# Kernel tuning notes

Measured on AMD Instinct MI355X. Metric: run time of the kernel, lower is better.

The kernel has to match this reference:

```python
import jax, jax.numpy as jnp
import numpy as np

NUM_CLASSES = 80
ANCHORS = np.array([[10,13],[16,30],[33,23],[30,61],[62,45],[59,119],[116,90],[156,198],[373,326]], np.float32)
MASK = [[0,1,2],[3,4,5],[6,7,8]]
STRIDES = [8, 16, 32]
MAX_OUT = 100      # max_output_size_per_class == max_total_size
IOU_THR = 0.45
SCORE_THR = 0.25
NMS_TOPK = 128     # per-class candidate pre-selection for greedy NMS (>= MAX_OUT)


def setup_inputs() -> dict:
    key = jax.random.key(0)
    k1, k2, k3 = jax.random.split(key, 3)
    B = 16
    C = 3 * (NUM_CLASSES + 5)  # 255
    return {
        'p3': jax.random.normal(k1, (B, 80, 80, C), jnp.float32),
        'p4': jax.random.normal(k2, (B, 40, 40, C), jnp.float32),
        'p5': jax.random.normal(k3, (B, 20, 20, C), jnp.float32),
    }


def _decode(logits, anchors, stride):
    # logits: [B,H,W,3*(nc+5)] -> boxes [B,H*W*3,4] (x1y1x2y2), obj [B,M], cls [B,M,nc]
    B, H, W, _ = logits.shape
    A = anchors.shape[0]
    x = logits.reshape(B, H, W, A, NUM_CLASSES + 5)
    xy = jax.nn.sigmoid(x[..., :2])
    wh_logit = x[..., 2:4]
    obj = jax.nn.sigmoid(x[..., 4])
    cls = jax.nn.sigmoid(x[..., 5:])
    gx, gy = jnp.meshgrid(jnp.arange(W, dtype=x.dtype), jnp.arange(H, dtype=x.dtype))
    grid = jnp.stack([gx, gy], axis=-1)[:, :, None, :]  # [H,W,1,2]
    ctr = (xy + grid) * stride
    wh = jnp.exp(wh_logit) * anchors  # [B,H,W,A,2]
    box = jnp.concatenate([ctr - wh / 2.0, ctr + wh / 2.0], axis=-1)
    return box.reshape(B, -1, 4), obj.reshape(B, -1), cls.reshape(B, -1, NUM_CLASSES)


def _pairwise_iou(b):
    # b: [K,4] x1y1x2y2 -> [K,K]
    area = (b[:, 2] - b[:, 0]) * (b[:, 3] - b[:, 1])
    lt = jnp.maximum(b[:, None, :2], b[None, :, :2])
    rb = jnp.minimum(b[:, None, 2:], b[None, :, 2:])
    wh = jnp.clip(rb - lt, 0.0)
    inter = wh[..., 0] * wh[..., 1]
    return inter / (area[:, None] + area[None, :] - inter + 1e-9)


def _nms_single(boxes, scores):
    # boxes [N,4], scores [N] for one (image, class): greedy NMS on top-K candidates
    s = jnp.where(scores > SCORE_THR, scores, -1.0)
    top_s, idx = jax.lax.top_k(s, NMS_TOPK)   # sorted descending
    b = boxes[idx]                            # [K,4]
    iou = _pairwise_iou(b)                    # [K,K]
    rng = jnp.arange(NMS_TOPK)

    def body(keep, i):
        active = keep[i] & (top_s[i] > 0.0)
        sup = active & (iou[i] > IOU_THR) & (rng > i)
        return keep & ~sup, None

    keep, _ = jax.lax.scan(body, jnp.ones(NMS_TOPK, bool), rng)
    valid = keep & (top_s > 0.0)
    ss = jnp.where(valid, top_s, -1.0)
    sel_s, sel_i = jax.lax.top_k(ss, MAX_OUT)
    return b[sel_i], sel_s                    # [M,4], [M]


def _per_image(boxes, scores_cn):
    # boxes [N,4] shared across classes (q=1), scores_cn [C,N]
    cb, cs = jax.vmap(_nms_single, in_axes=(None, 0))(boxes, scores_cn)  # [C,M,4],[C,M]
    C = cs.shape[0]
    cls_id = jnp.broadcast_to(jnp.arange(C, dtype=boxes.dtype)[:, None], cs.shape)
    fs, fi = jax.lax.top_k(cs.reshape(-1), MAX_OUT)
    fb = cb.reshape(-1, 4)[fi]
    fc = cls_id.reshape(-1)[fi]
    valid = fs > 0.0
    n_valid = jnp.sum(valid).astype(jnp.int32)
    return (jnp.where(valid[:, None], fb, 0.0),
            jnp.where(valid, fs, 0.0),
            jnp.where(valid, fc, 0.0),
            n_valid)


def _forward(p3, p4, p5):
    boxes, objs, clss = [], [], []
    for logits, m, stride in zip((p3, p4, p5), MASK, STRIDES):
        b, o, c = _decode(logits, jnp.asarray(ANCHORS[m]), float(stride))
        boxes.append(b); objs.append(o); clss.append(c)
    boxes = jnp.concatenate(boxes, axis=1)   # [B,N,4]
    obj = jnp.concatenate(objs, axis=1)      # [B,N]
    cls = jnp.concatenate(clss, axis=1)      # [B,N,C]
    scores = obj[..., None] * cls            # [B,N,C]
    return jax.vmap(_per_image)(boxes, scores.transpose(0, 2, 1))


def reference(p3, p4, p5):
    # returns (boxes [B,100,4], scores [B,100], classes [B,100], valid [B])
    return _forward(p3, p4, p5)
```

## Files before the change

kernel.cpp:

```cpp
#include <hip/hip_runtime.h>
#include <stdint.h>

#define NUM_CLASSES 80
#define N_ANCH 25200
#define B_IMG 16
#define NMS_TOPK_ 128
#define MAX_OUT_ 100
#define SCORE_THR_ 0.25f
#define IOU_THR_ 0.45f
#define NBINS 2048
#define CAP 2048
#define CAPB 1024
#define CAPC 256
#define U16_THR 0x3E80u
#define CHUNKS_PER_IMG 1575

__constant__ float c_anch[9][2] = {
    {10.f, 13.f}, {16.f, 30.f}, {33.f, 23.f},
    {30.f, 61.f}, {62.f, 45.f}, {59.f, 119.f},
    {116.f, 90.f}, {156.f, 198.f}, {373.f, 326.f}};

__device__ __forceinline__ float sigmoidf_(float x) {
    return 1.0f / (1.0f + expf(-x));
}

__device__ __forceinline__ unsigned int score_bin(unsigned int bits) {
    unsigned int bin = (bits - 0x3E800000u) >> 13;
    if (bin >= NBINS) bin = NBINS - 1;
    return bin;
}


__global__ void __launch_bounds__(256) decode_wave_kernel(
    const float* __restrict__ p3, const float* __restrict__ p4,
    const float* __restrict__ p5, float* __restrict__ boxes,
    unsigned short* __restrict__ score_u) {
    int wave = threadIdx.x >> 6;
    int lane = threadIdx.x & 63;
    int chunk = blockIdx.x * 4 + wave;
    int b = chunk / CHUNKS_PER_IMG;
    int ci = chunk - b * CHUNKS_PER_IMG;
    const float* p; int W, lvl, il0, base;
    if (ci < 1200)      { p = p3; W = 80; lvl = 0; il0 = ci * 16;          base = 0;     }
    else if (ci < 1500) { p = p4; W = 40; lvl = 1; il0 = (ci - 1200) * 16; base = 19200; }
    else                { p = p5; W = 20; lvl = 2; il0 = (ci - 1500) * 16; base = 24000; }
    float stride = (float)(8 << lvl);

    __shared__ float raw_s[4][16 * 85];
    __shared__ float obj_s[4][16];
    float* raw = raw_s[wave];
    float* obj_sh = obj_s[wave];

    {
        const float4* src4 = (const float4*)(p + (size_t)b * ((size_t)W * W * 255) +
                                             (size_t)il0 * 85);
        float4* raw4 = (float4*)raw;
#pragma unroll
        for (int k = 0; k < 6; ++k) {
            int idx = lane + k * 64;
            if (idx < 340) raw4[idx] = src4[idx];
        }
    }
    __threadfence_block();

    {
        int a = lane >> 2;
        int comp = lane & 3;
        int il = il0 + a;
        int y = il / (W * 3);
        int t = il - y * (W * 3);
        int x = t / 3;
        int an = t - x * 3;
        const float* q = &raw[a * 85];
        float cx = (sigmoidf_(q[0]) + (float)x) * stride;
        float cy = (sigmoidf_(q[1]) + (float)y) * stride;
        float bw = expf(q[2]) * c_anch[lvl * 3 + an][0];
        float bh = expf(q[3]) * c_anch[lvl * 3 + an][1];
        float v;
        if (comp == 0)      v = cx - bw * 0.5f;
        else if (comp == 1) v = cy - bh * 0.5f;
        else if (comp == 2) v = cx + bw * 0.5f;
        else                v = cy + bh * 0.5f;
        boxes[((size_t)b * N_ANCH + base + il) * 4 + comp] = v;
        if (comp == 0) obj_sh[a] = sigmoidf_(q[4]);
    }
    __threadfence_block();

    int gi0 = base + il0;
    int h = lane & 1;
    int c0 = lane >> 1;
    int j0 = h * 8;
#pragma unroll
    for (int it = 0; it < 3; ++it) {
        int c = it * 32 + c0;
        if (c < NUM_CLASSES) {
            unsigned int w[4];
#pragma unroll
            for (int k = 0; k < 4; ++k) {
                int j = j0 + 2 * k;
                float s0 = obj_sh[j]     * sigmoidf_(raw[j * 85 + 5 + c]);
                float s1 = obj_sh[j + 1] * sigmoidf_(raw[(j + 1) * 85 + 5 + c]);
                w[k] = (__float_as_uint(s0) >> 16) | (__float_as_uint(s1) & 0xFFFF0000u);
            }
            uint4 v = {w[0], w[1], w[2], w[3]};
            *(uint4*)(score_u + ((size_t)(b * NUM_CLASSES + c)) * N_ANCH + gi0 + j0) = v;
        }
    }
}

__global__ void __launch_bounds__(256) select_topk_u16_kernel(
    const unsigned short* __restrict__ score_u,
    const float* __restrict__ p3, const float* __restrict__ p4,
    const float* __restrict__ p5,
    unsigned long long* __restrict__ topsel) {
    int bc = blockIdx.x;
    int b = bc / NUM_CLASSES;
    int c = bc - b * NUM_CLASSES;
    int tid = threadIdx.x;
    int wave = tid >> 6;
    const uint4* sc = (const uint4*)(score_u + (size_t)bc * N_ANCH);

    __shared__ unsigned int hist[4][256];
    __shared__ unsigned long long sel[CAPB];
    __shared__ unsigned int s_cnt;
    __shared__ int s_cut;

#pragma unroll
    for (int wv = 0; wv < 4; ++wv) hist[wv][tid & 255] = 0u;
    if (tid == 0) s_cnt = 0u;
    __syncthreads();

    unsigned int* myhist = hist[wave];
    for (int i = tid; i < N_ANCH / 8; i += 256) {
        uint4 v = sc[i];
        unsigned int ww[4] = {v.x, v.y, v.z, v.w};
#pragma unroll
        for (int k = 0; k < 8; ++k) {
            unsigned int hh = (ww[k >> 1] >> ((k & 1) * 16)) & 0xFFFFu;
            if (hh >= U16_THR) {
                unsigned int bin = hh - U16_THR;
                if (bin > 255u) bin = 255u;
                atomicAdd(&myhist[bin], 1u);
            }
        }
    }
    __syncthreads();

    {
        unsigned int m = hist[0][tid] + hist[1][tid] + hist[2][tid] + hist[3][tid];
        hist[0][tid] = m;
    }
    __syncthreads();

    if (tid == 0) {
        unsigned int tot = 0; int cut = 0;
        for (int t = 255; t >= 0; --t) {
            tot += hist[0][t];
            if (tot >= NMS_TOPK_) { cut = t; break; }
        }
        s_cut = cut;
    }
    __syncthreads();
    unsigned int cutoff = (unsigned int)s_cut;

    for (int i = tid; i < N_ANCH / 8; i += 256) {
        uint4 v = sc[i];
        unsigned int ww[4] = {v.x, v.y, v.z, v.w};
#pragma unroll
        for (int k = 0; k < 8; ++k) {
            unsigned int hh = (ww[k >> 1] >> ((k & 1) * 16)) & 0xFFFFu;
            if (hh >= U16_THR) {
                unsigned int bin = hh - U16_THR;
                if (bin > 255u) bin = 255u;
                if (bin >= cutoff) {
                    unsigned int pos = atomicAdd(&s_cnt, 1u);
                    if (pos < CAPB) sel[pos] = (unsigned long long)(i * 8 + k);
                }
            }
        }
    }
    __syncthreads();

    unsigned int M = s_cnt;
    if (M > CAPB) M = CAPB;

    for (unsigned int t = tid; t < M; t += 256) {
        unsigned int idx = (unsigned int)sel[t];
        const float* q;
        if (idx < 19200u)      q = p3 + (size_t)b * 1632000 + (size_t)idx * 85;
        else if (idx < 24000u) q = p4 + (size_t)b * 408000 + (size_t)(idx - 19200u) * 85;
        else                   q = p5 + (size_t)b * 102000 + (size_t)(idx - 24000u) * 85;
        float s = sigmoidf_(q[4]) * sigmoidf_(q[5 + c]);
        sel[t] = (s > SCORE_THR_)
                     ? (((unsigned long long)__float_as_uint(s) << 32) |
                        (unsigned long long)(~idx))
                     : 0ull;
    }
    __syncthreads();

    unsigned int P2 = 1;
    while (P2 < M) P2 <<= 1;
    if (P2 < 2) P2 = 2;
    for (unsigned int k = M + tid; k < P2; k += 256) sel[k] = 0ull;
    __syncthreads();

    for (unsigned int k = 2; k <= P2; k <<= 1) {
        for (unsigned int j = k >> 1; j > 0; j >>= 1) {
            for (unsigned int t = tid; t < (int)P2; t += 256) {
                unsigned int ixj = (unsigned int)t ^ j;
                if (ixj > (unsigned int)t) {
                    unsigned long long a0 = sel[t], b0 = sel[ixj];
                    bool desc = (((unsigned int)t & k) == 0);
                    if (desc ? (a0 < b0) : (a0 > b0)) { sel[t] = b0; sel[ixj] = a0; }
                }
            }
            __syncthreads();
        }
    }

    unsigned long long* dst = topsel + (size_t)bc * NMS_TOPK_;
    if (tid < NMS_TOPK_) dst[tid] = ((unsigned int)tid < M) ? sel[tid] : 0ull;
}

__global__ void __launch_bounds__(64) nms_kernel(
    const unsigned long long* __restrict__ topsel,
    const float* __restrict__ boxes,
    float* __restrict__ cls_score, float* __restrict__ cls_box) {
    int bc = blockIdx.x;
    int b = bc / NUM_CLASSES;
    unsigned int lane = threadIdx.x;

    __shared__ float bx[NMS_TOPK_][8];

    const unsigned long long* src = topsel + (size_t)bc * NMS_TOPK_;
    unsigned long long e0 = src[lane];
    unsigned long long e1 = src[64 + lane];

    bool k0 = (e0 != 0ull);
    bool k1 = (e1 != 0ull);

    float x00 = 0, y00 = 0, x01 = 0, y01 = 0, a0 = 0, sv0 = 0;
    float x10 = 0, y10 = 0, x11 = 0, y11 = 0, a1 = 0, sv1 = 0;
    if (k0) {
        unsigned int idx = ~((unsigned int)(e0 & 0xFFFFFFFFull));
        float4 bp = *(const float4*)(boxes + ((size_t)b * N_ANCH + idx) * 4);
        x00 = bp.x; y00 = bp.y; x01 = bp.z; y01 = bp.w;
        sv0 = __uint_as_float((unsigned int)(e0 >> 32));
        a0 = (x01 - x00) * (y01 - y00);
    }
    if (k1) {
        unsigned int idx = ~((unsigned int)(e1 & 0xFFFFFFFFull));
        float4 bp = *(const float4*)(boxes + ((size_t)b * N_ANCH + idx) * 4);
        x10 = bp.x; y10 = bp.y; x11 = bp.z; y11 = bp.w;
        sv1 = __uint_as_float((unsigned int)(e1 >> 32));
        a1 = (x11 - x10) * (y11 - y10);
    }
    {
        float4 v0 = {x00, y00, x01, y01};
        float4 v1 = {x10, y10, x11, y11};
        *(float4*)&bx[lane][0] = v0;
        *(float4*)&bx[64 + lane][0] = v1;
    }
    __syncthreads();

    unsigned long long km0 = __ballot(k0);
    unsigned long long km1 = __ballot(k1);
    for (unsigned int i = 0; i < NMS_TOPK_; ++i) {
        bool ki = ((((i < 64) ? km0 : km1) >> (i & 63)) & 1ull) != 0ull;
        if (ki) {
            float4 rb = *(const float4*)&bx[i][0];
            float ra = (rb.z - rb.x) * (rb.w - rb.y);
            if (k0 && lane > i) {
                float lx = fmaxf(rb.x, x00), ly = fmaxf(rb.y, y00);
                float rx = fminf(rb.z, x01), ry = fminf(rb.w, y01);
                float w = fmaxf(rx - lx, 0.f), h = fmaxf(ry - ly, 0.f);
                float inter = w * h;
                float iou = inter / (ra + a0 - inter + 1e-9f);
                if (iou > IOU_THR_) k0 = false;
            }
            if (k1 && (64 + lane) > i) {
                float lx = fmaxf(rb.x, x10), ly = fmaxf(rb.y, y10);
                float rx = fminf(rb.z, x11), ry = fminf(rb.w, y11);
                float w = fmaxf(rx - lx, 0.f), h = fmaxf(ry - ly, 0.f);
                float inter = w * h;
                float iou = inter / (ra + a1 - inter + 1e-9f);
                if (iou > IOU_THR_) k1 = false;
            }
            km0 = __ballot(k0);
            km1 = __ballot(k1);
        }
    }

    float* scd = cls_score + (size_t)bc * MAX_OUT_;
    float* bod = cls_box + (size_t)bc * (MAX_OUT_ * 4);
    int n0 = __popcll(km0);
    int n = n0 + __popcll(km1);
    if (k0) {
        int pos = __popcll(km0 & ((1ull << lane) - 1ull));
        if (pos < MAX_OUT_) {
            scd[pos] = sv0;
            bod[pos * 4 + 0] = x00; bod[pos * 4 + 1] = y00;
            bod[pos * 4 + 2] = x01; bod[pos * 4 + 3] = y01;
        }
    }
    if (k1) {
        int pos = n0 + __popcll(km1 & ((1ull << lane) - 1ull));
        if (pos < MAX_OUT_) {
            scd[pos] = sv1;
            bod[pos * 4 + 0] = x10; bod[pos * 4 + 1] = y10;
            bod[pos * 4 + 2] = x11; bod[pos * 4 + 3] = y11;
        }
    }
    int start = n < MAX_OUT_ ? n : MAX_OUT_;
    for (int p2 = start + (int)lane; p2 < MAX_OUT_; p2 += 64) {
        scd[p2] = -1.0f;
        bod[p2 * 4 + 0] = 0.f; bod[p2 * 4 + 1] = 0.f;
        bod[p2 * 4 + 2] = 0.f; bod[p2 * 4 + 3] = 0.f;
    }
}

__global__ void __launch_bounds__(256) final_fast_kernel(
    const float* __restrict__ cls_score, const float* __restrict__ cls_box,
    float* __restrict__ out) {
    int b = blockIdx.x;
    int tid = threadIdx.x;
    const int NC = NUM_CLASSES * MAX_OUT_;
    const float* sc = cls_score + (size_t)b * NC;

    __shared__ unsigned int hist[NBINS];
    __shared__ unsigned int segsum[256];
    __shared__ unsigned long long keys[CAPC];
    __shared__ unsigned int s_cnt, s_tot;
    __shared__ int s_cut;

    for (int k = tid; k < NBINS; k += 256) hist[k] = 0u;
    if (tid == 0) s_cnt = 0u;
    __syncthreads();

    for (int k = tid; k < NC; k += 256) {
        float s = sc[k];
        if (s > 0.0f) atomicAdd(&hist[score_bin(__float_as_uint(s))], 1u);
    }
    __syncthreads();

    unsigned int ss = 0;
    for (int k = 0; k < 8; ++k) ss += hist[tid * 8 + k];
    segsum[tid] = ss;
    __syncthreads();
    if (tid == 0) {
        unsigned int total = 0;
        for (int t = 0; t < 256; ++t) total += segsum[t];
        s_tot = total;
        unsigned int tot = 0; int cut = 0; int t = 255;
        for (; t >= 0; --t) {
            if (tot + segsum[t] >= MAX_OUT_) break;
            tot += segsum[t];
        }
        if (t >= 0) {
            int j = 7;
            for (; j >= 0; --j) { tot += hist[t * 8 + j]; if (tot >= MAX_OUT_) break; }
            if (j < 0) j = 0;
            cut = t * 8 + j;
        }
        s_cut = cut;
    }
    __syncthreads();
    unsigned int cutoff = (unsigned int)s_cut;

    for (int k = tid; k < NC; k += 256) {
        float s = sc[k];
        if (s > 0.0f && score_bin(__float_as_uint(s)) >= cutoff) {
            unsigned int pos = atomicAdd(&s_cnt, 1u);
            if (pos < CAPC) {
                keys[pos] = ((unsigned long long)__float_as_uint(s) << 32) |
                            (unsigned long long)(~(unsigned int)k);
            }
        }
    }
    __syncthreads();

    unsigned int M = s_cnt;
    if (M > CAPC) M = CAPC;
    unsigned int P2 = 1;
    while (P2 < M) P2 <<= 1;
    if (P2 < 2) P2 = 2;
    for (unsigned int k = M + tid; k < P2; k += 256) keys[k] = 0ull;
    __syncthreads();

    for (unsigned int k = 2; k <= P2; k <<= 1) {
        for (unsigned int j = k >> 1; j > 0; j >>= 1) {
            for (unsigned int t = (unsigned int)tid; t < P2; t += 256) {
                unsigned int ixj = t ^ j;
                if (ixj > t) {
                    unsigned long long a0 = keys[t], b0 = keys[ixj];
                    bool desc = ((t & k) == 0);
                    if (desc ? (a0 < b0) : (a0 > b0)) { keys[t] = b0; keys[ixj] = a0; }
                }
            }
            __syncthreads();
        }
    }

    float* ob = out;
    float* os = out + B_IMG * MAX_OUT_ * 4;
    float* oc = os + B_IMG * MAX_OUT_;
    float* on = oc + B_IMG * MAX_OUT_;

    unsigned int K = M < MAX_OUT_ ? M : MAX_OUT_;
    if (tid < MAX_OUT_) {
        if ((unsigned int)tid < K) {
            unsigned long long kk = keys[tid];
            unsigned int flat = ~((unsigned int)(kk & 0xFFFFFFFFull));
            float sv = __uint_as_float((unsigned int)(kk >> 32));
            const float* bp = cls_box + ((size_t)b * NC + flat) * 4;
            os[b * MAX_OUT_ + tid] = sv;
            oc[b * MAX_OUT_ + tid] = (float)(flat / MAX_OUT_);
            ob[(b * MAX_OUT_ + tid) * 4 + 0] = bp[0];
            ob[(b * MAX_OUT_ + tid) * 4 + 1] = bp[1];
            ob[(b * MAX_OUT_ + tid) * 4 + 2] = bp[2];
            ob[(b * MAX_OUT_ + tid) * 4 + 3] = bp[3];
        } else {
            os[b * MAX_OUT_ + tid] = 0.0f;
            oc[b * MAX_OUT_ + tid] = 0.0f;
            ob[(b * MAX_OUT_ + tid) * 4 + 0] = 0.0f;
            ob[(b * MAX_OUT_ + tid) * 4 + 1] = 0.0f;
            ob[(b * MAX_OUT_ + tid) * 4 + 2] = 0.0f;
            ob[(b * MAX_OUT_ + tid) * 4 + 3] = 0.0f;
        }
    }
    if (tid == 0) {
        unsigned int nv = s_tot < MAX_OUT_ ? s_tot : MAX_OUT_;
        on[b] = (float)nv;
    }
}


__global__ void __launch_bounds__(256) decode_kernel(
    const float* __restrict__ p3, const float* __restrict__ p4,
    const float* __restrict__ p5, float* __restrict__ boxes,
    float* __restrict__ obj) {
    int gid = blockIdx.x * blockDim.x + threadIdx.x;
    if (gid >= B_IMG * N_ANCH) return;
    int b = gid / N_ANCH;
    int i = gid - b * N_ANCH;
    const float* p; int W, il, lvl; float stride;
    if (i < 19200)      { p = p3; W = 80; il = i;         lvl = 0; stride = 8.f;  }
    else if (i < 24000) { p = p4; W = 40; il = i - 19200; lvl = 1; stride = 16.f; }
    else                { p = p5; W = 20; il = i - 24000; lvl = 2; stride = 32.f; }
    int y = il / (W * 3);
    int t = il - y * W * 3;
    int x = t / 3;
    int a = t - x * 3;
    const float* q = p + ((((size_t)b * W + y) * W + x) * 255 + a * 85);
    float cx = (sigmoidf_(q[0]) + (float)x) * stride;
    float cy = (sigmoidf_(q[1]) + (float)y) * stride;
    float bw = expf(q[2]) * c_anch[lvl * 3 + a][0];
    float bh = expf(q[3]) * c_anch[lvl * 3 + a][1];
    float* bo = boxes + (size_t)gid * 4;
    bo[0] = cx - bw * 0.5f; bo[1] = cy - bh * 0.5f;
    bo[2] = cx + bw * 0.5f; bo[3] = cy + bh * 0.5f;
    obj[gid] = sigmoidf_(q[4]);
}

__device__ __forceinline__ float cand_score(
    const float* __restrict__ p3, const float* __restrict__ p4,
    const float* __restrict__ p5, const float* __restrict__ obj,
    int b, int c, int i) {
    const float* p; int W, il;
    if (i < 19200)      { p = p3; W = 80; il = i;         }
    else if (i < 24000) { p = p4; W = 40; il = i - 19200; }
    else                { p = p5; W = 20; il = i - 24000; }
    int y = il / (W * 3);
    int t = il - y * W * 3;
    int x = t / 3;
    int a = t - x * 3;
    float cl = p[(((size_t)b * W + y) * W + x) * 255 + a * 85 + 5 + c];
    return obj[b * N_ANCH + i] * sigmoidf_(cl);
}

__global__ void __launch_bounds__(256) topk_nms_kernel(
    const float* __restrict__ p3, const float* __restrict__ p4,
    const float* __restrict__ p5, const float* __restrict__ boxes,
    const float* __restrict__ obj, float* __restrict__ cls_score,
    float* __restrict__ cls_box) {
    int b = blockIdx.x / NUM_CLASSES;
    int c = blockIdx.x % NUM_CLASSES;
    int tid = threadIdx.x;

    __shared__ unsigned int hist[NBINS];
    __shared__ unsigned long long keys[CAP];
    __shared__ unsigned int s_cnt, s_cutoff;
    __shared__ float bx[NMS_TOPK_][5];
    __shared__ float bs[NMS_TOPK_];
    __shared__ int keep[NMS_TOPK_];

    for (int k = tid; k < NBINS; k += 256) hist[k] = 0u;
    if (tid == 0) s_cnt = 0u;
    __syncthreads();

    for (int i = tid; i < N_ANCH; i += 256) {
        float s = cand_score(p3, p4, p5, obj, b, c, i);
        if (s > SCORE_THR_) atomicAdd(&hist[score_bin(__float_as_uint(s))], 1u);
    }
    __syncthreads();

    if (tid == 0) {
        unsigned int total = 0;
        int cut = 0;
        for (int k = NBINS - 1; k >= 0; --k) {
            total += hist[k];
            if (total >= NMS_TOPK_) { cut = k; break; }
        }
        s_cutoff = (unsigned int)cut;
    }
    __syncthreads();
    unsigned int cutoff = s_cutoff;

    for (int i = tid; i < N_ANCH; i += 256) {
        float s = cand_score(p3, p4, p5, obj, b, c, i);
        if (s > SCORE_THR_) {
            unsigned int bits = __float_as_uint(s);
            if (score_bin(bits) >= cutoff) {
                unsigned int pos = atomicAdd(&s_cnt, 1u);
                if (pos < CAP) {
                    keys[pos] = ((unsigned long long)bits << 32) |
                                (unsigned long long)(~(unsigned int)i);
                }
            }
        }
    }
    __syncthreads();

    unsigned int M = s_cnt;
    if (M > CAP) M = CAP;
    unsigned int P2 = 1;
    while (P2 < M) P2 <<= 1;
    if (P2 < 2) P2 = 2;
    for (unsigned int k = M + tid; k < P2; k += 256) keys[k] = 0ull;
    __syncthreads();

    for (unsigned int k = 2; k <= P2; k <<= 1) {
        for (unsigned int j = k >> 1; j > 0; j >>= 1) {
            for (unsigned int t = tid; t < P2; t += 256) {
                unsigned int ixj = t ^ j;
                if (ixj > t) {
                    unsigned long long a0 = keys[t], b0 = keys[ixj];
                    bool desc = ((t & k) == 0);
                    if (desc ? (a0 < b0) : (a0 > b0)) { keys[t] = b0; keys[ixj] = a0; }
                }
            }
            __syncthreads();
        }
    }

    unsigned int K = M < NMS_TOPK_ ? M : NMS_TOPK_;
    if (tid < (int)K) {
        unsigned long long kk = keys[tid];
        unsigned int idx = ~((unsigned int)(kk & 0xFFFFFFFFull));
        const float* bp = boxes + ((size_t)b * N_ANCH + idx) * 4;
        bx[tid][0] = bp[0]; bx[tid][1] = bp[1];
        bx[tid][2] = bp[2]; bx[tid][3] = bp[3];
        bs[tid] = __uint_as_float((unsigned int)(kk >> 32));
        keep[tid] = 1;
    }
    __syncthreads();

    for (unsigned int i = 0; i < K; ++i) {
        if (keep[i]) {
            unsigned int t = (unsigned int)tid;
            if (t > i && t < K && keep[t]) {
                float ax0 = bx[i][0], ay0 = bx[i][1], ax1 = bx[i][2], ay1 = bx[i][3];
                float cx0 = bx[t][0], cy0 = bx[t][1], cx1 = bx[t][2], cy1 = bx[t][3];
                float areaA = (ax1 - ax0) * (ay1 - ay0);
                float areaB = (cx1 - cx0) * (cy1 - cy0);
                float lx = fmaxf(ax0, cx0), ly = fmaxf(ay0, cy0);
                float rx = fminf(ax1, cx1), ry = fminf(ay1, cy1);
                float w = rx - lx; if (w < 0.f) w = 0.f;
                float h = ry - ly; if (h < 0.f) h = 0.f;
                float inter = w * h;
                float iou = inter / (areaA + areaB - inter + 1e-9f);
                if (iou > IOU_THR_) keep[t] = 0;
            }
        }
        __syncthreads();
    }

    if (tid == 0) {
        float* scd = cls_score + ((size_t)b * NUM_CLASSES + c) * MAX_OUT_;
        float* bod = cls_box + ((size_t)b * NUM_CLASSES + c) * MAX_OUT_ * 4;
        int out_n = 0;
        for (unsigned int t2 = 0; t2 < K && out_n < MAX_OUT_; ++t2) {
            if (keep[t2]) {
                scd[out_n] = bs[t2];
                bod[out_n * 4 + 0] = bx[t2][0];
                bod[out_n * 4 + 1] = bx[t2][1];
                bod[out_n * 4 + 2] = bx[t2][2];
                bod[out_n * 4 + 3] = bx[t2][3];
                out_n++;
            }
        }
        for (; out_n < MAX_OUT_; ++out_n) {
            scd[out_n] = -1.0f;
            bod[out_n * 4 + 0] = 0.f; bod[out_n * 4 + 1] = 0.f;
            bod[out_n * 4 + 2] = 0.f; bod[out_n * 4 + 3] = 0.f;
        }
    }
}

extern "C" void kernel_launch(void* const* d_in, const int* in_sizes, int n_in,
                              void* d_out, int out_size, void* d_ws, size_t ws_size,
                              hipStream_t stream) {
    const float* p3 = (const float*)d_in[0];
    const float* p4 = (const float*)d_in[1];
    const float* p5 = (const float*)d_in[2];

    const size_t boxesB  = (size_t)B_IMG * N_ANCH * 4 * sizeof(float);
    const size_t clsSB   = (size_t)B_IMG * NUM_CLASSES * MAX_OUT_ * sizeof(float);
    const size_t clsBB   = clsSB * 4;
    const size_t topselB = (size_t)B_IMG * NUM_CLASSES * NMS_TOPK_ * 8;
    const size_t scoreUB = (size_t)B_IMG * NUM_CLASSES * N_ANCH * 2;
    const size_t need_new = boxesB + clsSB + clsBB + topselB + scoreUB;

    char* base = (char*)d_ws;

    if (ws_size >= need_new) {
        float* boxes     = (float*)base;
        float* cls_score = (float*)(base + boxesB);
        float* cls_box   = (float*)(base + boxesB + clsSB);
        unsigned long long* topsel =
            (unsigned long long*)(base + boxesB + clsSB + clsBB);
        unsigned short* score_u =
            (unsigned short*)(base + boxesB + clsSB + clsBB + topselB);

        decode_wave_kernel<<<(B_IMG * CHUNKS_PER_IMG) / 4, 256, 0, stream>>>(
            p3, p4, p5, boxes, score_u);
        select_topk_u16_kernel<<<B_IMG * NUM_CLASSES, 256, 0, stream>>>(
            score_u, p3, p4, p5, topsel);
        nms_kernel<<<B_IMG * NUM_CLASSES, 64, 0, stream>>>(
            topsel, boxes, cls_score, cls_box);
        final_fast_kernel<<<B_IMG, 256, 0, stream>>>(cls_score, cls_box, (float*)d_out);
    } else {
        float* boxes = (float*)base;
        float* obj = boxes + (size_t)B_IMG * N_ANCH * 4;
        float* cls_score = obj + (size_t)B_IMG * N_ANCH;
        float* cls_box = cls_score + (size_t)B_IMG * NUM_CLASSES * MAX_OUT_;

        int tot = B_IMG * N_ANCH;
        decode_kernel<<<(tot + 255) / 256, 256, 0, stream>>>(p3, p4, p5, boxes, obj);
        topk_nms_kernel<<<B_IMG * NUM_CLASSES, 256, 0, stream>>>(
            p3, p4, p5, boxes, obj, cls_score, cls_box);
        final_fast_kernel<<<B_IMG, 256, 0, stream>>>(cls_score, cls_box, (float*)d_out);
    }
}
```

Before: 310.2 us.

## Quantize per-class score cache to 8-bit bins and use fast sigmoid

Replaces the 16-bit truncated score cache with an 8-bit bin code (the top float bits offset from a base, clamped), which halves the intermediate score buffer written by decode and read twice by the top-k selection kernel. Box decoding now has one lane per anchor writing a float4 instead of four lanes each writing a scalar. Class scores use a fast exp/divide sigmoid, and each lane handles one class across all 16 anchors. Selection collects candidates from one bin below the cutoff to absorb the coarser quantization, then rescoring from the raw logits keeps exact ordering, at the risk of more candidates or CAPB overflow when bins are coarse.

```diff
diff --git a/kernel.cpp b/kernel.cpp
--- a/kernel.cpp
+++ b/kernel.cpp
@@ -12,7 +12,7 @@
 #define CAP 2048
 #define CAPB 1024
 #define CAPC 256
-#define U16_THR 0x3E80u
+#define U8_BASE 0x3E7Eu
 #define CHUNKS_PER_IMG 1575
 
 __constant__ float c_anch[9][2] = {
@@ -24,6 +24,19 @@
     return 1.0f / (1.0f + expf(-x));
 }
 
+__device__ __forceinline__ float fast_sigmoid_(float x) {
+    float t = __expf(-x);
+    return __fdividef(1.0f, 1.0f + t);
+}
+
+__device__ __forceinline__ unsigned int score_u8_(float s) {
+    unsigned int u = __float_as_uint(s) >> 16;
+    int bin = (int)u - (int)U8_BASE;
+    if (bin < 0) bin = 0;
+    if (bin > 255) bin = 255;
+    return (unsigned int)bin;
+}
+
 __device__ __forceinline__ unsigned int score_bin(unsigned int bits) {
     unsigned int bin = (bits - 0x3E800000u) >> 13;
     if (bin >= NBINS) bin = NBINS - 1;
@@ -34,7 +47,7 @@
 __global__ void __launch_bounds__(256) decode_wave_kernel(
     const float* __restrict__ p3, const float* __restrict__ p4,
     const float* __restrict__ p5, float* __restrict__ boxes,
-    unsigned short* __restrict__ score_u) {
+    unsigned char* __restrict__ score_u8) {
     int wave = threadIdx.x >> 6;
     int lane = threadIdx.x & 63;
     int chunk = blockIdx.x * 4 + wave;
@@ -63,9 +76,8 @@
     }
     __threadfence_block();
 
-    {
-        int a = lane >> 2;
-        int comp = lane & 3;
+    if (lane < 16) {
+        int a = lane;
         int il = il0 + a;
         int y = il / (W * 3);
         int t = il - y * (W * 3);
@@ -76,40 +88,38 @@
         float cy = (sigmoidf_(q[1]) + (float)y) * stride;
         float bw = expf(q[2]) * c_anch[lvl * 3 + an][0];
         float bh = expf(q[3]) * c_anch[lvl * 3 + an][1];
-        float v;
-        if (comp == 0)      v = cx - bw * 0.5f;
-        else if (comp == 1) v = cy - bh * 0.5f;
-        else if (comp == 2) v = cx + bw * 0.5f;
-        else                v = cy + bh * 0.5f;
-        boxes[((size_t)b * N_ANCH + base + il) * 4 + comp] = v;
-        if (comp == 0) obj_sh[a] = sigmoidf_(q[4]);
+        float4 bo = {cx - bw * 0.5f, cy - bh * 0.5f,
+                     cx + bw * 0.5f, cy + bh * 0.5f};
+        *(float4*)(boxes + ((size_t)b * N_ANCH + base + il) * 4) = bo;
+        obj_sh[a] = fast_sigmoid_(q[4]);
     }
     __threadfence_block();
 
-    int gi0 = base + il0;
-    int h = lane & 1;
-    int c0 = lane >> 1;
-    int j0 = h * 8;
+    size_t rowbase = (size_t)b * NUM_CLASSES * N_ANCH + (size_t)(base + il0);
 #pragma unroll
-    for (int it = 0; it < 3; ++it) {
-        int c = it * 32 + c0;
+    for (int it = 0; it < 2; ++it) {
+        int c = it * 64 + lane;
         if (c < NUM_CLASSES) {
             unsigned int w[4];
 #pragma unroll
-            for (int k = 0; k < 4; ++k) {
-                int j = j0 + 2 * k;
-                float s0 = obj_sh[j]     * sigmoidf_(raw[j * 85 + 5 + c]);
-                float s1 = obj_sh[j + 1] * sigmoidf_(raw[(j + 1) * 85 + 5 + c]);
-                w[k] = (__float_as_uint(s0) >> 16) | (__float_as_uint(s1) & 0xFFFF0000u);
+            for (int g = 0; g < 4; ++g) {
+                unsigned int acc = 0;
+#pragma unroll
+                for (int a4 = 0; a4 < 4; ++a4) {
+                    int a = g * 4 + a4;
+                    float s = obj_sh[a] * fast_sigmoid_(raw[a * 85 + 5 + c]);
+                    acc |= score_u8_(s) << (8 * a4);
+                }
+                w[g] = acc;
             }
             uint4 v = {w[0], w[1], w[2], w[3]};
-            *(uint4*)(score_u + ((size_t)(b * NUM_CLASSES + c)) * N_ANCH + gi0 + j0) = v;
-        }
-    }
-}
-
-__global__ void __launch_bounds__(256) select_topk_u16_kernel(
-    const unsigned short* __restrict__ score_u,
+            *(uint4*)(score_u8 + rowbase + (size_t)c * N_ANCH) = v;
+        }
+    }
+}
+
+__global__ void __launch_bounds__(256) select_topk_u8_kernel(
+    const unsigned char* __restrict__ score_u8,
     const float* __restrict__ p3, const float* __restrict__ p4,
     const float* __restrict__ p5,
     unsigned long long* __restrict__ topsel) {
@@ -118,7 +128,7 @@
     int c = bc - b * NUM_CLASSES;
     int tid = threadIdx.x;
     int wave = tid >> 6;
-    const uint4* sc = (const uint4*)(score_u + (size_t)bc * N_ANCH);
+    const uint4* sc = (const uint4*)(score_u8 + (size_t)bc * N_ANCH);
 
     __shared__ unsigned int hist[4][256];
     __shared__ unsigned long long sel[CAPB];
@@ -131,17 +141,13 @@
     __syncthreads();
 
     unsigned int* myhist = hist[wave];
-    for (int i = tid; i < N_ANCH / 8; i += 256) {
+    for (int i = tid; i < N_ANCH / 16; i += 256) {
         uint4 v = sc[i];
         unsigned int ww[4] = {v.x, v.y, v.z, v.w};
 #pragma unroll
-        for (int k = 0; k < 8; ++k) {
-            unsigned int hh = (ww[k >> 1] >> ((k & 1) * 16)) & 0xFFFFu;
-            if (hh >= U16_THR) {
-                unsigned int bin = hh - U16_THR;
-                if (bin > 255u) bin = 255u;
-                atomicAdd(&myhist[bin], 1u);
-            }
+        for (int k = 0; k < 16; ++k) {
+            unsigned int bin = (ww[k >> 2] >> ((k & 3) * 8)) & 0xFFu;
+            if (bin) atomicAdd(&myhist[bin], 1u);
         }
     }
     __syncthreads();
@@ -154,28 +160,25 @@
 
     if (tid == 0) {
         unsigned int tot = 0; int cut = 0;
-        for (int t = 255; t >= 0; --t) {
+        for (int t = 255; t >= 1; --t) {
             tot += hist[0][t];
             if (tot >= NMS_TOPK_) { cut = t; break; }
         }
         s_cut = cut;
     }
     __syncthreads();
-    unsigned int cutoff = (unsigned int)s_cut;
-
-    for (int i = tid; i < N_ANCH / 8; i += 256) {
+    int coll = s_cut - 1;
+    if (coll < 1) coll = 1;
+
+    for (int i = tid; i < N_ANCH / 16; i += 256) {
         uint4 v = sc[i];
         unsigned int ww[4] = {v.x, v.y, v.z, v.w};
 #pragma unroll
-        for (int k = 0; k < 8; ++k) {
-            unsigned int hh = (ww[k >> 1] >> ((k & 1) * 16)) & 0xFFFFu;
-            if (hh >= U16_THR) {
-                unsigned int bin = hh - U16_THR;
-                if (bin > 255u) bin = 255u;
-                if (bin >= cutoff) {
-                    unsigned int pos = atomicAdd(&s_cnt, 1u);
-                    if (pos < CAPB) sel[pos] = (unsigned long long)(i * 8 + k);
-                }
+        for (int k = 0; k < 16; ++k) {
+            unsigned int bin = (ww[k >> 2] >> ((k & 3) * 8)) & 0xFFu;
+            if ((int)bin >= coll) {
+                unsigned int pos = atomicAdd(&s_cnt, 1u);
+                if (pos < CAPB) sel[pos] = (unsigned long long)(i * 16 + k);
             }
         }
     }
@@ -618,7 +621,7 @@
     const size_t clsSB   = (size_t)B_IMG * NUM_CLASSES * MAX_OUT_ * sizeof(float);
     const size_t clsBB   = clsSB * 4;
     const size_t topselB = (size_t)B_IMG * NUM_CLASSES * NMS_TOPK_ * 8;
-    const size_t scoreUB = (size_t)B_IMG * NUM_CLASSES * N_ANCH * 2;
+    const size_t scoreUB = (size_t)B_IMG * NUM_CLASSES * N_ANCH;
     const size_t need_new = boxesB + clsSB + clsBB + topselB + scoreUB;
 
     char* base = (char*)d_ws;
@@ -629,13 +632,13 @@
         float* cls_box   = (float*)(base + boxesB + clsSB);
         unsigned long long* topsel =
             (unsigned long long*)(base + boxesB + clsSB + clsBB);
-        unsigned short* score_u =
-            (unsigned short*)(base + boxesB + clsSB + clsBB + topselB);
+        unsigned char* score_u8 =
+            (unsigned char*)(base + boxesB + clsSB + clsBB + topselB);
 
         decode_wave_kernel<<<(B_IMG * CHUNKS_PER_IMG) / 4, 256, 0, stream>>>(
-            p3, p4, p5, boxes, score_u);
-        select_topk_u16_kernel<<<B_IMG * NUM_CLASSES, 256, 0, stream>>>(
-            score_u, p3, p4, p5, topsel);
+            p3, p4, p5, boxes, score_u8);
+        select_topk_u8_kernel<<<B_IMG * NUM_CLASSES, 256, 0, stream>>>(
+            score_u8, p3, p4, p5, topsel);
         nms_kernel<<<B_IMG * NUM_CLASSES, 64, 0, stream>>>(
             topsel, boxes, cls_score, cls_box);
         final_fast_kernel<<<B_IMG, 256, 0, stream>>>(cls_score, cls_box, (float*)d_out);
```

Measured after the change: 298.1 us. 1.04x faster.
